# Kernel tuning notes

Hardware: AMD Instinct MI355X
Metric: run time of the kernel (lower is better)

## Reference

```python
import jax, jax.numpy as jnp
import numpy as np

N_NODES = 25000
N_EDGES = 400000
D_FEAT = 128
HIDDEN = 64
HEADS = 4


def _segment_softmax(logits, segment_ids, num_segments):
    # numerically stable softmax over variable-size neighborhoods
    seg_max = jax.ops.segment_max(logits, segment_ids, num_segments=num_segments)
    ex = jnp.exp(logits - seg_max[segment_ids])
    seg_sum = jax.ops.segment_sum(ex, segment_ids, num_segments=num_segments)
    return ex / seg_sum[segment_ids]


def _gat_layer(nodes, senders, receivers, Wq, bq, Wl, bl, last):
    n = nodes.shape[0]
    h = (nodes @ Wq + bq)[:, :, None]            # [N, hidden, 1] (query fn + expand_dims)
    sent = h[senders]                            # [E, hidden, 1]
    recv = h[receivers]                          # [E, hidden, 1]
    cat = jnp.concatenate([sent, recv], axis=-1) # [E, hidden, 2]
    logits = jax.nn.leaky_relu(cat @ Wl + bl, negative_slope=0.2)  # [E, hidden, heads]
    w = _segment_softmax(logits, receivers, n)   # [E, hidden, heads]
    msgs = sent * w                              # broadcast over heads
    agg = jax.ops.segment_sum(msgs, receivers, num_segments=n)     # [N, hidden, heads]
    if last:
        return jax.nn.elu(agg.mean(axis=-1))     # [N, hidden]
    return jax.nn.elu(agg.reshape(n, -1))        # [N, hidden*heads]


def setup_inputs() -> dict:
    key = jax.random.key(0)
    ks = jax.random.split(key, 16)
    d1 = HIDDEN * HEADS
    inp = {
        "nodes": jax.random.normal(ks[0], (N_NODES, D_FEAT), dtype=jnp.float32),
        "senders": jax.random.randint(ks[1], (N_EDGES,), 0, N_NODES, dtype=jnp.int64)
        if jax.config.jax_enable_x64 else jax.random.randint(ks[1], (N_EDGES,), 0, N_NODES).astype(jnp.int32),
        "receivers": jax.random.randint(ks[2], (N_EDGES,), 0, N_NODES).astype(jnp.int32),
        "Wq0": jax.random.normal(ks[3], (D_FEAT, HIDDEN), dtype=jnp.float32) / np.sqrt(D_FEAT),
        "bq0": jnp.zeros((HIDDEN,), jnp.float32),
        "Wl0": jax.random.normal(ks[4], (2, HEADS), dtype=jnp.float32) / np.sqrt(2.0),
        "bl0": jnp.zeros((HEADS,), jnp.float32),
        "Wq1": jax.random.normal(ks[5], (d1, HIDDEN), dtype=jnp.float32) / np.sqrt(d1),
        "bq1": jnp.zeros((HIDDEN,), jnp.float32),
        "Wl1": jax.random.normal(ks[6], (2, HEADS), dtype=jnp.float32) / np.sqrt(2.0),
        "bl1": jnp.zeros((HEADS,), jnp.float32),
        "Wq2": jax.random.normal(ks[7], (d1, HIDDEN), dtype=jnp.float32) / np.sqrt(d1),
        "bq2": jnp.zeros((HIDDEN,), jnp.float32),
        "Wl2": jax.random.normal(ks[8], (2, HEADS), dtype=jnp.float32) / np.sqrt(2.0),
        "bl2": jnp.zeros((HEADS,), jnp.float32),
    }
    inp["senders"] = inp["senders"].astype(jnp.int32)
    return inp


def reference(nodes, senders, receivers, Wq0, bq0, Wl0, bl0, Wq1, bq1, Wl1, bl1, Wq2, bq2, Wl2, bl2):
    x = _gat_layer(nodes, senders, receivers, Wq0, bq0, Wl0, bl0, last=False)
    x = _gat_layer(x, senders, receivers, Wq1, bq1, Wl1, bl1, last=False)
    x = _gat_layer(x, senders, receivers, Wq2, bq2, Wl2, bl2, last=True)
    return x
```

## Files before the change

### kernel.cpp

```cpp
#include <hip/hip_runtime.h>
#include <hip/hip_bf16.h>

#define HID 64
#define HEADS 4

typedef short s16x8 __attribute__((ext_vector_type(8)));
typedef short s16x4 __attribute__((ext_vector_type(4)));
typedef float f32x4 __attribute__((ext_vector_type(4)));
typedef float f32x2 __attribute__((ext_vector_type(2)));

__device__ __forceinline__ float ldw(const void* p, long i, bool f32) {
    return f32 ? ((const float*)p)[i] : (float)((const __hip_bfloat16*)p)[i];
}

__device__ __forceinline__ unsigned short f2b(float f) {
    unsigned int u = __builtin_bit_cast(unsigned int, f);
    u += 0x7FFF + ((u >> 16) & 1);
    return (unsigned short)(u >> 16);
}
__device__ __forceinline__ float b2f(unsigned short s) {
    unsigned int u = ((unsigned int)s) << 16;
    return __builtin_bit_cast(float, u);
}
__device__ __forceinline__ short f2h(float f) {
    return __builtin_bit_cast(short, (_Float16)f);
}

#if __has_builtin(__builtin_amdgcn_exp2f)
#define EXP2(x) __builtin_amdgcn_exp2f(x)
#else
#define EXP2(x) exp2f(x)
#endif
#if __has_builtin(__builtin_amdgcn_rcpf)
#define RCP(x) __builtin_amdgcn_rcpf(x)
#else
#define RCP(x) (1.0f / (x))
#endif

__global__ __launch_bounds__(256) void prep_kernel(
    const void* __restrict__ nodes,
    const void* __restrict__ W0, const void* __restrict__ W1, const void* __restrict__ W2,
    const void* __restrict__ Wl0, const void* __restrict__ bl0,
    const void* __restrict__ Wl1, const void* __restrict__ bl1,
    const void* __restrict__ Wl2, const void* __restrict__ bl2,
    int* __restrict__ flag_out,
    unsigned short* __restrict__ T0, unsigned short* __restrict__ T1,
    unsigned short* __restrict__ T2, float* __restrict__ Wlp) {
    __shared__ int sflag;
    if (threadIdx.x == 0) sflag = 0;
    __syncthreads();
    {
        const uint4* pw = (const uint4*)nodes;
        int hits = 0;
        for (int i = threadIdx.x; i < 2048; i += 256) {
            uint4 u = pw[i];
            unsigned int w[4] = {u.x, u.y, u.z, u.w};
            #pragma unroll
            for (int j = 0; j < 4; j++) {
                if ((w[j] & 0x7F80u) == 0x7F80u) hits++;
                if (((w[j] >> 16) & 0x7F80u) == 0x7F80u) hits++;
            }
        }
        if (__ballot(hits != 0)) { if ((threadIdx.x & 63) == 0) sflag = 1; }
    }
    __syncthreads();
    const bool f32 = (sflag != 0);
    if (blockIdx.x == 0 && threadIdx.x == 0) *flag_out = f32 ? 100 : 0;

    int g = blockIdx.x * 256 + threadIdx.x;
    int stride = gridDim.x * 256;

    for (int i = g; i < 40960; i += stride) {
        int k, n;
        if (i < 8192) {
            k = i >> 6; n = i & 63;
            T0[n * 128 + k] = f32 ? f2b(((const float*)W0)[i])
                                  : ((const unsigned short*)W0)[i];
        } else {
            const void* W; unsigned short* T; int o;
            if (i < 24576) { W = W1; T = T1; o = i - 8192; }
            else           { W = W2; T = T2; o = i - 24576; }
            k = o >> 6; n = o & 63;
            float w = ldw(W, o, f32);
            T[n * 256 + k] = f32 ? f2b(w) : (unsigned short)f2h(w);
        }
    }
    if (blockIdx.x == 0 && threadIdx.x < 48) {
        int L = threadIdx.x >> 4, s = threadIdx.x & 15;
        const void* W = (L == 0) ? Wl0 : ((L == 1) ? Wl1 : Wl2);
        const void* B = (L == 0) ? bl0 : ((L == 1) ? bl1 : bl2);
        float v = 0.f;
        if (s < 8)       v = ldw(W, s, f32);
        else if (s < 12) v = ldw(B, s - 8, f32);
        Wlp[L * 16 + s] = v * 1.44269504f;
    }
}

template <int K, int AMODE>
__device__ __forceinline__ void gemm_body(const unsigned short* __restrict__ Ah,
                                          const unsigned short* __restrict__ Al,
                                          const unsigned short* __restrict__ Wt,
                                          const void* __restrict__ bq,
                                          bool f32,
                                          _Float16* __restrict__ h, int M, int blockId) {
    constexpr int KP = K + 8;
    __shared__ __align__(16) unsigned short Ws[64 * KP];
    int tid = threadIdx.x;
    #pragma unroll
    for (int it = 0; it < (64 * K) / 2048; it++) {
        int i = it * 2048 + tid * 8;
        int row = i / K, col = i % K;
        *(s16x8*)&Ws[row * KP + col] = *(const s16x8*)(Wt + i);
    }
    __syncthreads();

    int lane = tid & 63, wv = tid >> 6;
    int m16 = lane & 15, quad = lane >> 4;

    int tiles = (M + 15) >> 4;
    int tile = blockId * 4 + wv;
    if (tile >= tiles) return;

    float bias[4];
    #pragma unroll
    for (int t = 0; t < 4; t++) bias[t] = ldw(bq, 16 * t + m16, f32);

    int m0 = tile << 4;
    int row = m0 + m16;
    bool rv = row < M;
    long abase = (long)row * K;
    f32x4 acc[4] = {{0.f,0.f,0.f,0.f},{0.f,0.f,0.f,0.f},{0.f,0.f,0.f,0.f},{0.f,0.f,0.f,0.f}};

    #pragma unroll
    for (int ks = 0; ks < K / 32; ks++) {
        int kb = ks * 32 + quad * 8;
        s16x8 b[4];
        #pragma unroll
        for (int t = 0; t < 4; t++)
            b[t] = *(const s16x8*)&Ws[(16 * t + m16) * KP + kb];
        if (AMODE == 3) {
            const float* Af = (const float*)Ah;
            f32x4 v0 = {0.f,0.f,0.f,0.f}, v1 = {0.f,0.f,0.f,0.f};
            if (rv) {
                v0 = *(const f32x4*)(Af + abase + kb);
                v1 = *(const f32x4*)(Af + abase + kb + 4);
            }
            s16x8 ah, al;
            #pragma unroll
            for (int jj = 0; jj < 8; jj++) {
                float f = (jj < 4) ? v0[jj] : v1[jj - 4];
                unsigned short hb = f2b(f);
                ah[jj] = (short)hb;
                al[jj] = (short)f2b(f - b2f(hb));
            }
            #pragma unroll
            for (int t = 0; t < 4; t++)
                acc[t] = __builtin_amdgcn_mfma_f32_16x16x32_bf16(ah, b[t], acc[t], 0, 0, 0);
            #pragma unroll
            for (int t = 0; t < 4; t++)
                acc[t] = __builtin_amdgcn_mfma_f32_16x16x32_bf16(al, b[t], acc[t], 0, 0, 0);
        } else {
            s16x8 ah = rv ? *(const s16x8*)(Ah + abase + kb) : (s16x8){0,0,0,0,0,0,0,0};
            if (AMODE == 0) {
                #pragma unroll
                for (int t = 0; t < 4; t++)
                    acc[t] = __builtin_amdgcn_mfma_f32_16x16x32_bf16(ah, b[t], acc[t], 0, 0, 0);
            } else if (AMODE == 1) {
                #pragma unroll
                for (int t = 0; t < 4; t++)
                    acc[t] = __builtin_amdgcn_mfma_f32_16x16x32_f16(ah, b[t], acc[t], 0, 0, 0);
            } else {
                #pragma unroll
                for (int t = 0; t < 4; t++)
                    acc[t] = __builtin_amdgcn_mfma_f32_16x16x32_bf16(ah, b[t], acc[t], 0, 0, 0);
                s16x8 al = rv ? *(const s16x8*)(Al + abase + kb) : (s16x8){0,0,0,0,0,0,0,0};
                #pragma unroll
                for (int t = 0; t < 4; t++)
                    acc[t] = __builtin_amdgcn_mfma_f32_16x16x32_bf16(al, b[t], acc[t], 0, 0, 0);
            }
        }
    }

    #pragma unroll
    for (int t = 0; t < 4; t++) {
        #pragma unroll
        for (int r = 0; r < 4; r++) {
            int orow = m0 + quad * 4 + r;
            if (orow < M) h[(long)orow * 64 + 16 * t + m16] = (_Float16)(acc[t][r] + bias[t]);
        }
    }
}

template <int K>
__global__ __launch_bounds__(256) void gemm_mfma(const unsigned short* __restrict__ Ah,
                                                 const unsigned short* __restrict__ Al,
                                                 const unsigned short* __restrict__ Wt,
                                                 const void* __restrict__ bq,
                                                 const int* __restrict__ flag,
                                                 _Float16* __restrict__ h, int M) {
    const bool f32 = (*flag >= 8);
    if (f32) gemm_body<K, 2>(Ah, Al, Wt, bq, true, h, M, blockIdx.x);
    else     gemm_body<K, 1>(Ah, nullptr, Wt, bq, false, h, M, blockIdx.x);
}

__global__ __launch_bounds__(256) void gemm0_scatter(
    const void* __restrict__ nodes,
    const unsigned short* __restrict__ Wt, const void* __restrict__ bq,
    const int* __restrict__ flag, _Float16* __restrict__ h, int M,
    const int* __restrict__ recv, const int* __restrict__ send,
    int* __restrict__ cnt, int* __restrict__ slots, int E, int gemmBlocks) {
    if ((int)blockIdx.x < gemmBlocks) {
        const bool f32 = (*flag >= 8);
        if (f32) gemm_body<128, 3>((const unsigned short*)nodes, nullptr, Wt, bq,
                                   true, h, M, blockIdx.x);
        else     gemm_body<128, 0>((const unsigned short*)nodes, nullptr, Wt, bq,
                                   false, h, M, blockIdx.x);
    } else {
        int g = (blockIdx.x - gemmBlocks) * 256 + threadIdx.x;
        int stride = (gridDim.x - gemmBlocks) * 256;
        for (int i = g; i < E; i += stride) {
            int r = recv[i];
            int pos = atomicAdd(&cnt[r], 1);
            if (pos < 64) slots[r * 64 + pos] = send[i] * HID;
        }
    }
}

__global__ __launch_bounds__(256) void attn_kernel(
    const _Float16* __restrict__ h, const int* __restrict__ cnt,
    const int* __restrict__ slots,
    const float* __restrict__ wlp,
    const int* __restrict__ flag,
    unsigned short* __restrict__ xh, unsigned short* __restrict__ xl,
    void* __restrict__ out, int n, int last) {
    const bool f32 = (*flag >= 8);
    int lane = threadIdx.x & 63;
    int r = __builtin_amdgcn_readfirstlane(blockIdx.x * 4 + (threadIdx.x >> 6));
    if (r >= n) return;

    int cR = cnt[r];
    cR = min(cR, 64);
    int sv = slots[r * 64 + lane];
    if (lane >= cR) sv = 0;

    float hr = (float)h[(long)r * HID + lane];
    f32x4 w0v = *(const f32x4*)(wlp);
    f32x4 w1v = *(const f32x4*)(wlp + 4);
    f32x4 bv  = *(const f32x4*)(wlp + 8);
    f32x2 w0p[2], cp[2];
    #pragma unroll
    for (int q = 0; q < 2; q++) {
        #pragma unroll
        for (int c = 0; c < 2; c++) {
            int k = 2 * q + c;
            w0p[q][c] = w0v[k];
            cp[q][c] = fmaf(hr, w1v[k], bv[k]);
        }
    }

    f32x2 lp[2] = {{0.f, 0.f}, {0.f, 0.f}};
    f32x2 ap[2] = {{0.f, 0.f}, {0.f, 0.f}};
    const _Float16* hbp = h + lane;

    #define LD(j) hbp[(long)__builtin_amdgcn_readlane(sv, (j))]
    #define STEP(hc) {                                                     \
        float _h = (float)(hc);                       \
        _Pragma("unroll")                                                  \
        for (int q = 0; q < 2; q++) {                                      \
            f32x2 t = w0p[q] * _h + cp[q];                                 \
            f32x2 u = t * 0.2f;                                            \
            t.x = fmaxf(t.x, u.x); t.y = fmaxf(t.y, u.y);                  \
            f32x2 pe; pe.x = EXP2(t.x); pe.y = EXP2(t.y);                  \
            lp[q] += pe;                                                   \
            ap[q] += pe * _h;                                              \
        } }

    _Float16 q0 = LD(0), q1 = LD(1), q2 = LD(2), q3 = LD(3);
    _Float16 q4 = LD(4), q5 = LD(5), q6 = LD(6), q7 = LD(7);
    int j = 0;
    for (; j + 8 <= cR; j += 8) {
        _Float16 a0 = q0, a1 = q1, a2 = q2, a3 = q3;
        _Float16 a4 = q4, a5 = q5, a6 = q6, a7 = q7;
        if (j + 8 < 64) {
            q0 = LD(j +  8); q1 = LD(j +  9); q2 = LD(j + 10); q3 = LD(j + 11);
            q4 = LD(j + 12); q5 = LD(j + 13); q6 = LD(j + 14); q7 = LD(j + 15);
        }
        STEP(a0); STEP(a1); STEP(a2); STEP(a3);
        STEP(a4); STEP(a5); STEP(a6); STEP(a7);
    }
    int remn = cR - j;
    if (remn > 0) STEP(q0);
    if (remn > 1) STEP(q1);
    if (remn > 2) STEP(q2);
    if (remn > 3) STEP(q3);
    if (remn > 4) STEP(q4);
    if (remn > 5) STEP(q5);
    if (remn > 6) STEP(q6);
    #undef LD
    #undef STEP

    bool has = (cR > 0);
    if (!last) {
        float v[4];
        #pragma unroll
        for (int k = 0; k < HEADS; k++) {
            float a = has ? ap[k >> 1][k & 1] * RCP(lp[k >> 1][k & 1]) : 0.f;
            v[k] = (a > 0.f) ? a : (__expf(a) - 1.f);
        }
        long o = (long)r * (HID * HEADS) + lane * HEADS;
        if (!f32) {
            s16x4 vf;
            #pragma unroll
            for (int k = 0; k < HEADS; k++) vf[k] = f2h(v[k]);
            *(s16x4*)(xh + o) = vf;
        } else {
            s16x4 vh, vlo;
            #pragma unroll
            for (int k = 0; k < HEADS; k++) {
                unsigned short hbk = f2b(v[k]);
                vh[k] = (short)hbk;
                vlo[k] = (short)f2b(v[k] - b2f(hbk));
            }
            *(s16x4*)(xh + o) = vh;
            *(s16x4*)(xl + o) = vlo;
        }
    } else {
        float s = 0.f;
        #pragma unroll
        for (int k = 0; k < HEADS; k++)
            s += has ? ap[k >> 1][k & 1] * RCP(lp[k >> 1][k & 1]) : 0.f;
        float a = s * 0.25f;
        a = (a > 0.f) ? a : (__expf(a) - 1.f);
        if (f32) ((float*)out)[(long)r * HID + lane] = a;
        else     ((__hip_bfloat16*)out)[(long)r * HID + lane] = (__hip_bfloat16)a;
    }
}


extern "C" void kernel_launch(void* const* d_in, const int* in_sizes, int n_in,
                              void* d_out, int out_size, void* d_ws, size_t ws_size,
                              hipStream_t stream) {
    const void* nodes    = d_in[0];
    const int* senders   = (const int*)d_in[1];
    const int* receivers = (const int*)d_in[2];
    const void* Wq0 = d_in[3];  const void* bq0 = d_in[4];
    const void* Wl0 = d_in[5];  const void* bl0 = d_in[6];
    const void* Wq1 = d_in[7];  const void* bq1 = d_in[8];
    const void* Wl1 = d_in[9];  const void* bl1 = d_in[10];
    const void* Wq2 = d_in[11]; const void* bq2 = d_in[12];
    const void* Wl2 = d_in[13]; const void* bl2 = d_in[14];

    int N = in_sizes[0] / 128;
    int E = in_sizes[1];

    char* p = (char*)d_ws;
    int* flag = (int*)p;            p += 64;
    _Float16* h = (_Float16*)p;     p += (size_t)N * 64 * 2;
    unsigned short* xh = (unsigned short*)p;  p += (size_t)N * 256 * 2;
    unsigned short* xl = (unsigned short*)p;  p += (size_t)N * 256 * 2;
    unsigned short* Wt0 = (unsigned short*)p; p += 128 * 64 * 2;
    unsigned short* Wt1 = (unsigned short*)p; p += 256 * 64 * 2;
    unsigned short* Wt2 = (unsigned short*)p; p += 256 * 64 * 2;
    float* Wlp = (float*)p;         p += 64 * 4;
    int* cnt = (int*)p;             p += (((size_t)N + 63) / 64) * 64 * 4;
    int* slots = (int*)p;           p += (size_t)N * 64 * 4;

    hipMemsetAsync(cnt, 0, (size_t)N * sizeof(int), stream);

    prep_kernel<<<64, 256, 0, stream>>>(nodes, Wq0, Wq1, Wq2,
                                        Wl0, bl0, Wl1, bl1, Wl2, bl2,
                                        flag, Wt0, Wt1, Wt2, Wlp);

    int attnGrid = (N + 3) / 4;
    int tiles = (N + 15) / 16;
    int gemmGrid = (tiles + 3) / 4;

    gemm0_scatter<<<gemmGrid * 2, 256, 0, stream>>>(nodes, Wt0, bq0, flag, h, N,
                                                    receivers, senders, cnt, slots,
                                                    E, gemmGrid);
    attn_kernel<<<attnGrid, 256, 0, stream>>>(h, cnt, slots, Wlp + 0, flag,
                                              xh, xl, nullptr, N, 0);
    gemm_mfma<256><<<gemmGrid, 256, 0, stream>>>(xh, xl, Wt1, bq1, flag, h, N);
    attn_kernel<<<attnGrid, 256, 0, stream>>>(h, cnt, slots, Wlp + 16, flag,
                                              xh, xl, nullptr, N, 0);
    gemm_mfma<256><<<gemmGrid, 256, 0, stream>>>(xh, xl, Wt2, bq2, flag, h, N);
    attn_kernel<<<attnGrid, 256, 0, stream>>>(h, cnt, slots, Wlp + 32, flag,
                                              nullptr, nullptr, d_out, N, 1);
}
```

Baseline: 217.9 us.

## Fuse attention aggregation with next-layer GEMM and fold count reset into prep

Adds an attn_gemm kernel in which each 64-thread block aggregates 16 receiver rows with the edge softmax, keeps the resulting 16x256 features in shared memory, and multiplies them by the next layer's weights with MFMA. This removes the round trip of the xh intermediate through global memory and two kernel launches. The cnt memset moves into prep_kernel. In exchange, each one-wave block now runs its 16 rows one after another, so parallelism and latency hiding differ from the old 4-wave attention kernel, and the next row's loads are prefetched to partly cover that.

```diff
diff --git a/kernel.cpp b/kernel.cpp
--- a/kernel.cpp
+++ b/kernel.cpp
@@ -37,6 +37,48 @@
 #define RCP(x) (1.0f / (x))
 #endif
 
+__device__ __forceinline__ void edge_softmax(
+    const _Float16* __restrict__ hbp, int sv, int cR,
+    const f32x2 (&w0p)[2], const f32x2 (&cp)[2],
+    f32x2 (&lp)[2], f32x2 (&ap)[2]) {
+    #define LD(j) hbp[(long)__builtin_amdgcn_readlane(sv, (j))]
+    #define STEP(hc) {                                                     \
+        float _h = (float)(hc);                       \
+        _Pragma("unroll")                                                  \
+        for (int q = 0; q < 2; q++) {                                      \
+            f32x2 t = w0p[q] * _h + cp[q];                                 \
+            f32x2 u = t * 0.2f;                                            \
+            t.x = fmaxf(t.x, u.x); t.y = fmaxf(t.y, u.y);                  \
+            f32x2 pe; pe.x = EXP2(t.x); pe.y = EXP2(t.y);                  \
+            lp[q] += pe;                                                   \
+            ap[q] += pe * _h;                                              \
+        } }
+
+    _Float16 q0 = LD(0), q1 = LD(1), q2 = LD(2), q3 = LD(3);
+    _Float16 q4 = LD(4), q5 = LD(5), q6 = LD(6), q7 = LD(7);
+    int j = 0;
+    for (; j + 8 <= cR; j += 8) {
+        _Float16 a0 = q0, a1 = q1, a2 = q2, a3 = q3;
+        _Float16 a4 = q4, a5 = q5, a6 = q6, a7 = q7;
+        if (j + 8 < 64) {
+            q0 = LD(j +  8); q1 = LD(j +  9); q2 = LD(j + 10); q3 = LD(j + 11);
+            q4 = LD(j + 12); q5 = LD(j + 13); q6 = LD(j + 14); q7 = LD(j + 15);
+        }
+        STEP(a0); STEP(a1); STEP(a2); STEP(a3);
+        STEP(a4); STEP(a5); STEP(a6); STEP(a7);
+    }
+    int remn = cR - j;
+    if (remn > 0) STEP(q0);
+    if (remn > 1) STEP(q1);
+    if (remn > 2) STEP(q2);
+    if (remn > 3) STEP(q3);
+    if (remn > 4) STEP(q4);
+    if (remn > 5) STEP(q5);
+    if (remn > 6) STEP(q6);
+    #undef LD
+    #undef STEP
+}
+
 __global__ __launch_bounds__(256) void prep_kernel(
     const void* __restrict__ nodes,
     const void* __restrict__ W0, const void* __restrict__ W1, const void* __restrict__ W2,
@@ -45,7 +87,8 @@
     const void* __restrict__ Wl2, const void* __restrict__ bl2,
     int* __restrict__ flag_out,
     unsigned short* __restrict__ T0, unsigned short* __restrict__ T1,
-    unsigned short* __restrict__ T2, float* __restrict__ Wlp) {
+    unsigned short* __restrict__ T2, float* __restrict__ Wlp,
+    int* __restrict__ cnt, int N64) {
     __shared__ int sflag;
     if (threadIdx.x == 0) sflag = 0;
     __syncthreads();
@@ -69,6 +112,8 @@
 
     int g = blockIdx.x * 256 + threadIdx.x;
     int stride = gridDim.x * 256;
+
+    for (int i = g; i < N64; i += stride) cnt[i] = 0;
 
     for (int i = g; i < 40960; i += stride) {
         int k, n;
@@ -98,7 +143,6 @@
 
 template <int K, int AMODE>
 __device__ __forceinline__ void gemm_body(const unsigned short* __restrict__ Ah,
-                                          const unsigned short* __restrict__ Al,
                                           const unsigned short* __restrict__ Wt,
                                           const void* __restrict__ bq,
                                           bool f32,
@@ -161,23 +205,9 @@
                 acc[t] = __builtin_amdgcn_mfma_f32_16x16x32_bf16(al, b[t], acc[t], 0, 0, 0);
         } else {
             s16x8 ah = rv ? *(const s16x8*)(Ah + abase + kb) : (s16x8){0,0,0,0,0,0,0,0};
-            if (AMODE == 0) {
-                #pragma unroll
-                for (int t = 0; t < 4; t++)
-                    acc[t] = __builtin_amdgcn_mfma_f32_16x16x32_bf16(ah, b[t], acc[t], 0, 0, 0);
-            } else if (AMODE == 1) {
-                #pragma unroll
-                for (int t = 0; t < 4; t++)
-                    acc[t] = __builtin_amdgcn_mfma_f32_16x16x32_f16(ah, b[t], acc[t], 0, 0, 0);
-            } else {
-                #pragma unroll
-                for (int t = 0; t < 4; t++)
-                    acc[t] = __builtin_amdgcn_mfma_f32_16x16x32_bf16(ah, b[t], acc[t], 0, 0, 0);
-                s16x8 al = rv ? *(const s16x8*)(Al + abase + kb) : (s16x8){0,0,0,0,0,0,0,0};
-                #pragma unroll
-                for (int t = 0; t < 4; t++)
-                    acc[t] = __builtin_amdgcn_mfma_f32_16x16x32_bf16(al, b[t], acc[t], 0, 0, 0);
-            }
+            #pragma unroll
+            for (int t = 0; t < 4; t++)
+                acc[t] = __builtin_amdgcn_mfma_f32_16x16x32_bf16(ah, b[t], acc[t], 0, 0, 0);
         }
     }
 
@@ -189,18 +219,6 @@
             if (orow < M) h[(long)orow * 64 + 16 * t + m16] = (_Float16)(acc[t][r] + bias[t]);
         }
     }
-}
-
-template <int K>
-__global__ __launch_bounds__(256) void gemm_mfma(const unsigned short* __restrict__ Ah,
-                                                 const unsigned short* __restrict__ Al,
-                                                 const unsigned short* __restrict__ Wt,
-                                                 const void* __restrict__ bq,
-                                                 const int* __restrict__ flag,
-                                                 _Float16* __restrict__ h, int M) {
-    const bool f32 = (*flag >= 8);
-    if (f32) gemm_body<K, 2>(Ah, Al, Wt, bq, true, h, M, blockIdx.x);
-    else     gemm_body<K, 1>(Ah, nullptr, Wt, bq, false, h, M, blockIdx.x);
 }
 
 __global__ __launch_bounds__(256) void gemm0_scatter(
@@ -211,9 +229,9 @@
     int* __restrict__ cnt, int* __restrict__ slots, int E, int gemmBlocks) {
     if ((int)blockIdx.x < gemmBlocks) {
         const bool f32 = (*flag >= 8);
-        if (f32) gemm_body<128, 3>((const unsigned short*)nodes, nullptr, Wt, bq,
+        if (f32) gemm_body<128, 3>((const unsigned short*)nodes, Wt, bq,
                                    true, h, M, blockIdx.x);
-        else     gemm_body<128, 0>((const unsigned short*)nodes, nullptr, Wt, bq,
+        else     gemm_body<128, 0>((const unsigned short*)nodes, Wt, bq,
                                    false, h, M, blockIdx.x);
     } else {
         int g = (blockIdx.x - gemmBlocks) * 256 + threadIdx.x;
@@ -226,13 +244,132 @@
     }
 }
 
+#define XKP 264
+template <int WORLD>
+__device__ __forceinline__ void ag_body(
+    const _Float16* __restrict__ h, const int* __restrict__ cnt,
+    const int* __restrict__ slots, const float* __restrict__ wlp,
+    const unsigned short* __restrict__ Wt, const void* __restrict__ bq,
+    unsigned short* __restrict__ xl, _Float16* __restrict__ hout,
+    int M, unsigned short* __restrict__ Xs) {
+    int lane = threadIdx.x & 63;
+    long base = (long)blockIdx.x * 16;
+
+    f32x4 w0v = *(const f32x4*)(wlp);
+    f32x4 w1v = *(const f32x4*)(wlp + 4);
+    f32x4 bv  = *(const f32x4*)(wlp + 8);
+    int cv = cnt[base + (lane & 15)];
+    const _Float16* hbp = h + lane;
+
+    int sv_n = slots[base * 64 + lane];
+    _Float16 hr_n = h[base * 64 + lane];
+
+    #pragma unroll 1
+    for (int i = 0; i < 16; i++) {
+        int cR = __builtin_amdgcn_readlane(cv, i);
+        cR = min(cR, 64);
+        int svc = sv_n;
+        float hrc = (float)hr_n;
+        long rn = base + ((i < 15) ? i + 1 : 15);
+        sv_n = slots[rn * 64 + lane];
+        hr_n = h[rn * 64 + lane];
+        if (lane >= cR) svc = 0;
+
+        f32x2 w0p[2], cp[2];
+        #pragma unroll
+        for (int q = 0; q < 2; q++) {
+            #pragma unroll
+            for (int c = 0; c < 2; c++) {
+                int k = 2 * q + c;
+                w0p[q][c] = w0v[k];
+                cp[q][c] = fmaf(hrc, w1v[k], bv[k]);
+            }
+        }
+        f32x2 lp[2] = {{0.f, 0.f}, {0.f, 0.f}};
+        f32x2 ap[2] = {{0.f, 0.f}, {0.f, 0.f}};
+        edge_softmax(hbp, svc, cR, w0p, cp, lp, ap);
+
+        bool has = (cR > 0);
+        float v[4];
+        #pragma unroll
+        for (int k = 0; k < HEADS; k++) {
+            float a = has ? ap[k >> 1][k & 1] * RCP(lp[k >> 1][k & 1]) : 0.f;
+            v[k] = (a > 0.f) ? a : (__expf(a) - 1.f);
+        }
+        if (WORLD == 0) {
+            s16x4 vf;
+            #pragma unroll
+            for (int k = 0; k < HEADS; k++) vf[k] = f2h(v[k]);
+            *(s16x4*)&Xs[i * XKP + lane * 4] = vf;
+        } else {
+            s16x4 vh, vlo;
+            #pragma unroll
+            for (int k = 0; k < HEADS; k++) {
+                unsigned short hbk = f2b(v[k]);
+                vh[k] = (short)hbk;
+                vlo[k] = (short)f2b(v[k] - b2f(hbk));
+            }
+            *(s16x4*)&Xs[i * XKP + lane * 4] = vh;
+            *(s16x4*)(xl + (base + i) * 256 + lane * 4) = vlo;
+        }
+    }
+
+    int m16 = lane & 15, quad = lane >> 4;
+    float bias[4];
+    #pragma unroll
+    for (int t = 0; t < 4; t++) bias[t] = ldw(bq, 16 * t + m16, WORLD == 1);
+    f32x4 acc[4] = {{0.f,0.f,0.f,0.f},{0.f,0.f,0.f,0.f},{0.f,0.f,0.f,0.f},{0.f,0.f,0.f,0.f}};
+
+    #pragma unroll
+    for (int ks = 0; ks < 8; ks++) {
+        int kb = ks * 32 + quad * 8;
+        s16x8 b[4];
+        #pragma unroll
+        for (int t = 0; t < 4; t++)
+            b[t] = *(const s16x8*)(Wt + (16 * t + m16) * 256 + kb);
+        s16x8 ah = *(const s16x8*)&Xs[m16 * XKP + kb];
+        if (WORLD == 0) {
+            #pragma unroll
+            for (int t = 0; t < 4; t++)
+                acc[t] = __builtin_amdgcn_mfma_f32_16x16x32_f16(ah, b[t], acc[t], 0, 0, 0);
+        } else {
+            #pragma unroll
+            for (int t = 0; t < 4; t++)
+                acc[t] = __builtin_amdgcn_mfma_f32_16x16x32_bf16(ah, b[t], acc[t], 0, 0, 0);
+            s16x8 al = *(const s16x8*)(xl + (base + m16) * 256 + kb);
+            #pragma unroll
+            for (int t = 0; t < 4; t++)
+                acc[t] = __builtin_amdgcn_mfma_f32_16x16x32_bf16(al, b[t], acc[t], 0, 0, 0);
+        }
+    }
+
+    #pragma unroll
+    for (int t = 0; t < 4; t++) {
+        #pragma unroll
+        for (int r = 0; r < 4; r++) {
+            long orow = base + quad * 4 + r;
+            if (orow < M) hout[orow * 64 + 16 * t + m16] = (_Float16)(acc[t][r] + bias[t]);
+        }
+    }
+}
+
+__global__ __launch_bounds__(64, 4) void attn_gemm(
+    const _Float16* __restrict__ h, const int* __restrict__ cnt,
+    const int* __restrict__ slots, const float* __restrict__ wlp,
+    const unsigned short* __restrict__ Wt, const void* __restrict__ bq,
+    const int* __restrict__ flag,
+    unsigned short* __restrict__ xl, _Float16* __restrict__ hout, int M) {
+    __shared__ __align__(16) unsigned short Xs[16 * XKP];
+    if (*flag >= 8) ag_body<1>(h, cnt, slots, wlp, Wt, bq, xl, hout, M, Xs);
+    else            ag_body<0>(h, cnt, slots, wlp, Wt, bq, xl, hout, M, Xs);
+}
+
 __global__ __launch_bounds__(256) void attn_kernel(
     const _Float16* __restrict__ h, const int* __restrict__ cnt,
     const int* __restrict__ slots,
     const float* __restrict__ wlp,
     const int* __restrict__ flag,
-    unsigned short* __restrict__ xh, unsigned short* __restrict__ xl,
-    void* __restrict__ out, int n, int last) {
+    void* __restrict__ out, int n) {
     const bool f32 = (*flag >= 8);
     int lane = threadIdx.x & 63;
     int r = __builtin_amdgcn_readfirstlane(blockIdx.x * 4 + (threadIdx.x >> 6));
@@ -257,83 +394,19 @@
             cp[q][c] = fmaf(hr, w1v[k], bv[k]);
         }
     }
-
     f32x2 lp[2] = {{0.f, 0.f}, {0.f, 0.f}};
     f32x2 ap[2] = {{0.f, 0.f}, {0.f, 0.f}};
-    const _Float16* hbp = h + lane;
-
-    #define LD(j) hbp[(long)__builtin_amdgcn_readlane(sv, (j))]
-    #define STEP(hc) {                                                     \
-        float _h = (float)(hc);                       \
-        _Pragma("unroll")                                                  \
-        for (int q = 0; q < 2; q++) {                                      \
-            f32x2 t = w0p[q] * _h + cp[q];                                 \
-            f32x2 u = t * 0.2f;                                            \
-            t.x = fmaxf(t.x, u.x); t.y = fmaxf(t.y, u.y);                  \
-            f32x2 pe; pe.x = EXP2(t.x); pe.y = EXP2(t.y);                  \
-            lp[q] += pe;                                                   \
-            ap[q] += pe * _h;                                              \
-        } }
-
-    _Float16 q0 = LD(0), q1 = LD(1), q2 = LD(2), q3 = LD(3);
-    _Float16 q4 = LD(4), q5 = LD(5), q6 = LD(6), q7 = LD(7);
-    int j = 0;
-    for (; j + 8 <= cR; j += 8) {
-        _Float16 a0 = q0, a1 = q1, a2 = q2, a3 = q3;
-        _Float16 a4 = q4, a5 = q5, a6 = q6, a7 = q7;
-        if (j + 8 < 64) {
-            q0 = LD(j +  8); q1 = LD(j +  9); q2 = LD(j + 10); q3 = LD(j + 11);
-            q4 = LD(j + 12); q5 = LD(j + 13); q6 = LD(j + 14); q7 = LD(j + 15);
-        }
-        STEP(a0); STEP(a1); STEP(a2); STEP(a3);
-        STEP(a4); STEP(a5); STEP(a6); STEP(a7);
-    }
-    int remn = cR - j;
-    if (remn > 0) STEP(q0);
-    if (remn > 1) STEP(q1);
-    if (remn > 2) STEP(q2);
-    if (remn > 3) STEP(q3);
-    if (remn > 4) STEP(q4);
-    if (remn > 5) STEP(q5);
-    if (remn > 6) STEP(q6);
-    #undef LD
-    #undef STEP
+    edge_softmax(h + lane, sv, cR, w0p, cp, lp, ap);
 
     bool has = (cR > 0);
-    if (!last) {
-        float v[4];
-        #pragma unroll
-        for (int k = 0; k < HEADS; k++) {
-            float a = has ? ap[k >> 1][k & 1] * RCP(lp[k >> 1][k & 1]) : 0.f;
-            v[k] = (a > 0.f) ? a : (__expf(a) - 1.f);
-        }
-        long o = (long)r * (HID * HEADS) + lane * HEADS;
-        if (!f32) {
-            s16x4 vf;
-            #pragma unroll
-            for (int k = 0; k < HEADS; k++) vf[k] = f2h(v[k]);
-            *(s16x4*)(xh + o) = vf;
-        } else {
-            s16x4 vh, vlo;
-            #pragma unroll
-            for (int k = 0; k < HEADS; k++) {
-                unsigned short hbk = f2b(v[k]);
-                vh[k] = (short)hbk;
-                vlo[k] = (short)f2b(v[k] - b2f(hbk));
-            }
-            *(s16x4*)(xh + o) = vh;
-            *(s16x4*)(xl + o) = vlo;
-        }
-    } else {
-        float s = 0.f;
-        #pragma unroll
-        for (int k = 0; k < HEADS; k++)
-            s += has ? ap[k >> 1][k & 1] * RCP(lp[k >> 1][k & 1]) : 0.f;
-        float a = s * 0.25f;
-        a = (a > 0.f) ? a : (__expf(a) - 1.f);
-        if (f32) ((float*)out)[(long)r * HID + lane] = a;
-        else     ((__hip_bfloat16*)out)[(long)r * HID + lane] = (__hip_bfloat16)a;
-    }
+    float s = 0.f;
+    #pragma unroll
+    for (int k = 0; k < HEADS; k++)
+        s += has ? ap[k >> 1][k & 1] * RCP(lp[k >> 1][k & 1]) : 0.f;
+    float a = s * 0.25f;
+    a = (a > 0.f) ? a : (__expf(a) - 1.f);
+    if (f32) ((float*)out)[(long)r * HID + lane] = a;
+    else     ((__hip_bfloat16*)out)[(long)r * HID + lane] = (__hip_bfloat16)a;
 }
 
 
@@ -352,38 +425,36 @@
 
     int N = in_sizes[0] / 128;
     int E = in_sizes[1];
+    int N64 = ((N + 63) / 64) * 64;
 
     char* p = (char*)d_ws;
     int* flag = (int*)p;            p += 64;
-    _Float16* h = (_Float16*)p;     p += (size_t)N * 64 * 2;
-    unsigned short* xh = (unsigned short*)p;  p += (size_t)N * 256 * 2;
-    unsigned short* xl = (unsigned short*)p;  p += (size_t)N * 256 * 2;
+    _Float16* hA = (_Float16*)p;    p += (size_t)N64 * 64 * 2;
+    _Float16* hB = (_Float16*)p;    p += (size_t)N64 * 64 * 2;
+    unsigned short* xl = (unsigned short*)p;  p += (size_t)N64 * 256 * 2;
     unsigned short* Wt0 = (unsigned short*)p; p += 128 * 64 * 2;
     unsigned short* Wt1 = (unsigned short*)p; p += 256 * 64 * 2;
     unsigned short* Wt2 = (unsigned short*)p; p += 256 * 64 * 2;
     float* Wlp = (float*)p;         p += 64 * 4;
-    int* cnt = (int*)p;             p += (((size_t)N + 63) / 64) * 64 * 4;
-    int* slots = (int*)p;           p += (size_t)N * 64 * 4;
-
-    hipMemsetAsync(cnt, 0, (size_t)N * sizeof(int), stream);
+    int* cnt = (int*)p;             p += (size_t)N64 * 4;
+    int* slots = (int*)p;           p += (size_t)N64 * 64 * 4;
 
     prep_kernel<<<64, 256, 0, stream>>>(nodes, Wq0, Wq1, Wq2,
                                         Wl0, bl0, Wl1, bl1, Wl2, bl2,
-                                        flag, Wt0, Wt1, Wt2, Wlp);
-
-    int attnGrid = (N + 3) / 4;
+                                        flag, Wt0, Wt1, Wt2, Wlp, cnt, N64);
+
     int tiles = (N + 15) / 16;
     int gemmGrid = (tiles + 3) / 4;
-
-    gemm0_scatter<<<gemmGrid * 2, 256, 0, stream>>>(nodes, Wt0, bq0, flag, h, N,
+    int fGrid = N64 / 16;
+    int attnGrid = (N + 3) / 4;
+
+    gemm0_scatter<<<gemmGrid * 2, 256, 0, stream>>>(nodes, Wt0, bq0, flag, hA, N,
                                                     receivers, senders, cnt, slots,
                                                     E, gemmGrid);
-    attn_kernel<<<attnGrid, 256, 0, stream>>>(h, cnt, slots, Wlp + 0, flag,
-                                              xh, xl, nullptr, N, 0);
-    gemm_mfma<256><<<gemmGrid, 256, 0, stream>>>(xh, xl, Wt1, bq1, flag, h, N);
-    attn_kernel<<<attnGrid, 256, 0, stream>>>(h, cnt, slots, Wlp + 16, flag,
-                                              xh, xl, nullptr, N, 0);
-    gemm_mfma<256><<<gemmGrid, 256, 0, stream>>>(xh, xl, Wt2, bq2, flag, h, N);
-    attn_kernel<<<attnGrid, 256, 0, stream>>>(h, cnt, slots, Wlp + 32, flag,
-                                              nullptr, nullptr, d_out, N, 1);
-}
+    attn_gemm<<<fGrid, 64, 0, stream>>>(hA, cnt, slots, Wlp + 0, Wt1, bq1, flag,
+                                        xl, hB, N);
+    attn_gemm<<<fGrid, 64, 0, stream>>>(hB, cnt, slots, Wlp + 16, Wt2, bq2, flag,
+                                        xl, hA, N);
+    attn_kernel<<<attnGrid, 256, 0, stream>>>(hA, cnt, slots, Wlp + 32, flag,
+                                              d_out, N);
+}
```

New measurement: 240.3 us. +10.3%, slower.
